# Kernel tuning notes

Hardware: AMD Instinct MI355X
Metric: run time of the kernel (lower is better)

The kernel has to match this reference:

```python
import jax, jax.numpy as jnp
import numpy as np

N = 131072  # time steps
D = 4       # SDE state dimension


def setup_inputs() -> dict:
    key = jax.random.key(0)
    k = jax.random.split(key, 6)
    F = 0.1 * jax.random.normal(k[0], (D, D), jnp.float32)  # only shape/dtype used by filter
    H = jnp.zeros((1, D), jnp.float32).at[0, 0].set(1.0)    # observe first state component
    P_inf = jnp.eye(D, dtype=jnp.float32)
    # stable per-step transitions: spectral radius ~0.9
    A_seq = 0.9 * jnp.eye(D, dtype=jnp.float32)[None] + 0.02 * jax.random.normal(k[1], (N, D, D), jnp.float32)
    # PSD process noise per step
    S = 0.05 * jax.random.normal(k[2], (N, D, D), jnp.float32)
    Q_seq = jnp.einsum('nij,nkj->nik', S, S) + 1e-3 * jnp.eye(D, dtype=jnp.float32)[None]
    residual = jax.random.normal(k[3], (N,), jnp.float32)   # y - mean_fn(times)
    mask = jnp.ones((N,), jnp.float32)                      # all steps observed
    R_seq = 0.1 + 0.05 * jax.random.uniform(k[4], (N,), jnp.float32)  # noise_var + floor
    return dict(F=F, H=H, P_inf=P_inf, A_seq=A_seq, Q_seq=Q_seq,
                residual=residual, mask=mask, R_seq=R_seq)


def _kalman_filter(F, H, P_inf, A_seq, Q_seq, residual, mask, R_seq):
    d = F.shape[0]
    eye = jnp.eye(d, dtype=F.dtype)
    h = H[0]  # (d,)
    log_2pi = jnp.log(2.0 * jnp.pi).astype(F.dtype)

    def step(carry, inputs):
        m, P = carry
        A, Q, r_n, mask_n, R_n = inputs
        m_pred = A @ m
        P_pred = A @ P @ A.T + Q
        P_pred = 0.5 * (P_pred + P_pred.T)
        Ph = P_pred @ h                 # (d,)
        S = h @ Ph + R_n                # innovation variance
        innov = r_n - h @ m_pred
        is_obs = mask_n == 1
        S_safe = jnp.where(is_obs, S, 1.0)
        K = jnp.where(is_obs, Ph / S_safe, jnp.zeros_like(Ph))
        m_new = m_pred + K * innov
        I_KH = eye - K[:, None] * h[None, :]
        P_new = I_KH @ P_pred @ I_KH.T + R_n * (K[:, None] * K[None, :])
        P_new = 0.5 * (P_new + P_new.T)
        ll = jnp.where(is_obs, -0.5 * (log_2pi + jnp.log(S_safe) + innov * innov / S_safe), 0.0)
        return (m_new, P_new), (m_pred, P_pred, m_new, P_new, ll)

    m0 = jnp.zeros(d, dtype=F.dtype)
    _, (m_pred_seq, P_pred_seq, m_filt_seq, P_filt_seq, ll_seq) = jax.lax.scan(
        step, (m0, P_inf), (A_seq, Q_seq, residual, mask, R_seq))
    return m_pred_seq, P_pred_seq, m_filt_seq, P_filt_seq, jnp.sum(ll_seq)


def _rts_smoother(m_pred_seq, P_pred_seq, m_filt_seq, P_filt_seq, A_seq):
    def step(carry, inputs):
        m_ns, P_ns = carry
        m_f, P_f, m_pn, P_pn, A_n = inputs
        J = jnp.linalg.solve(P_pn.T, A_n @ P_f.T).T
        m_s = m_f + J @ (m_ns - m_pn)
        P_s = P_f + J @ (P_ns - P_pn) @ J.T
        P_s = 0.5 * (P_s + P_s.T)
        return (m_s, P_s), (m_s, P_s)

    m_T = m_filt_seq[-1]
    P_T = P_filt_seq[-1]
    inputs = (m_filt_seq[:-1], P_filt_seq[:-1], m_pred_seq[1:], P_pred_seq[1:], A_seq[1:])
    _, (m_s, P_s) = jax.lax.scan(step, (m_T, P_T), inputs, reverse=True)
    return (jnp.concatenate([m_s, m_T[None]], axis=0),
            jnp.concatenate([P_s, P_T[None]], axis=0))


def reference(F, H, P_inf, A_seq, Q_seq, residual, mask, R_seq):
    m_pred, P_pred, m_filt, P_filt, log_marginal = _kalman_filter(
        F, H, P_inf, A_seq, Q_seq, residual, mask, R_seq)
    m_smooth, P_smooth = _rts_smoother(m_pred, P_pred, m_filt, P_filt, A_seq)
    h = H[0]
    means = m_smooth @ h                                   # (N,) observation-space means
    vars_ = jnp.einsum('i,nij,j->n', h, P_smooth, h)       # (N,) marginal variances
    return means, vars_, log_marginal
```

## Files before the change

### kernel.cpp

```cpp
#include <hip/hip_runtime.h>
#include <math.h>

#define NN 131072
#define WUP 32
#define TPB 320
#define NOUT 256
#define NBLK (NN / NOUT)
#define WIN 321
#define NREC 288
#define LOG2PI 1.8378770664093453f

typedef __attribute__((ext_vector_type(2))) float f2;

__device__ double g_llb[NBLK];

__device__ __forceinline__ f2 bc(float s) {
  f2 r = {s, s};
  return r;
}
#define PF(a, b, c) __builtin_elementwise_fma((a), (b), (c))

__device__ __forceinline__ void ldpk_flat(const float4* s, int stride, int w, f2* M) {
#pragma unroll
  for (int c = 0; c < 4; ++c) {
    float4 v = s[c * stride + w];
    M[2 * c] = f2{v.x, v.y};
    M[2 * c + 1] = f2{v.z, v.w};
  }
}

__device__ __forceinline__ void sym_rows(const float4 t0, const float4 t1, const float2 t2,
                                         f2* M) {
  M[0] = f2{t0.x, t0.y};
  M[1] = f2{t0.z, t0.w};
  M[2] = f2{t0.y, t1.x};
  M[3] = f2{t1.y, t1.z};
  M[4] = f2{t0.z, t1.y};
  M[5] = f2{t1.w, t2.x};
  M[6] = f2{t0.w, t1.z};
  M[7] = f2{t2.x, t2.y};
}

__device__ __forceinline__ void kf_step_pk(const f2* __restrict__ AT, const f2* __restrict__ Q,
                                           float r, float mk, float R, f2* __restrict__ m,
                                           f2* __restrict__ P, float& Ss, float& innov,
                                           bool& obs) {
  float m0 = m[0][0], m1 = m[0][1], m2_ = m[1][0], m3 = m[1][1];
  f2 mp[2];
#pragma unroll
  for (int p = 0; p < 2; ++p) {
    f2 acc = AT[p] * bc(m0);
    acc = PF(bc(m1), AT[2 + p], acc);
    acc = PF(bc(m2_), AT[4 + p], acc);
    acc = PF(bc(m3), AT[6 + p], acc);
    mp[p] = acc;
  }

  f2 T[8];
#pragma unroll
  for (int i = 0; i < 4; ++i) {
    float a0 = AT[0 + (i >> 1)][i & 1];
    float a1 = AT[2 + (i >> 1)][i & 1];
    float a2 = AT[4 + (i >> 1)][i & 1];
    float a3 = AT[6 + (i >> 1)][i & 1];
#pragma unroll
    for (int p = 0; p < 2; ++p) {
      f2 acc = P[p] * bc(a0);
      acc = PF(bc(a1), P[2 + p], acc);
      acc = PF(bc(a2), P[4 + p], acc);
      acc = PF(bc(a3), P[6 + p], acc);
      T[2 * i + p] = acc;
    }
  }

  f2 Pp[8];
#pragma unroll
  for (int i = 0; i < 4; ++i) {
    float t0 = T[2 * i][0], t1 = T[2 * i][1], t2 = T[2 * i + 1][0], t3 = T[2 * i + 1][1];
#pragma unroll
    for (int p = 0; p < 2; ++p) {
      f2 acc = PF(bc(t0), AT[p], Q[2 * i + p]);
      acc = PF(bc(t1), AT[2 + p], acc);
      acc = PF(bc(t2), AT[4 + p], acc);
      acc = PF(bc(t3), AT[6 + p], acc);
      Pp[2 * i + p] = acc;
    }
  }

  float S = Pp[0][0] + R;
  innov = r - mp[0][0];
  obs = (mk == 1.0f);
  Ss = obs ? S : 1.0f;
  float kf = obs ? __builtin_amdgcn_rcpf(S) : 0.0f;
  f2 K[2] = {Pp[0] * bc(kf), Pp[1] * bc(kf)};
#pragma unroll
  for (int p = 0; p < 2; ++p) m[p] = PF(K[p], bc(innov), mp[p]);

#pragma unroll
  for (int i = 0; i < 4; ++i) {
    float Ki = K[i >> 1][i & 1];
#pragma unroll
    for (int p = 0; p < 2; ++p) P[2 * i + p] = PF(bc(-Ki), Pp[p], Pp[2 * i + p]);
  }
}

__device__ __forceinline__ void chol_solve_pk(const f2* __restrict__ S, const f2* __restrict__ T,
                                              f2* __restrict__ X) {
  float s00 = S[0][0];
  float s10 = S[2][0], s11 = S[2][1];
  float s20 = S[4][0], s21 = S[4][1], s22 = S[5][0];
  float s30 = S[6][0], s31 = S[6][1], s32 = S[7][0], s33 = S[7][1];
  float i00 = __builtin_amdgcn_rsqf(s00);
  float l10 = s10 * i00, l20 = s20 * i00, l30 = s30 * i00;
  float i11 = __builtin_amdgcn_rsqf(s11 - l10 * l10);
  float l21 = (s21 - l20 * l10) * i11;
  float l31 = (s31 - l30 * l10) * i11;
  float i22 = __builtin_amdgcn_rsqf(s22 - l20 * l20 - l21 * l21);
  float l32 = (s32 - l30 * l20 - l31 * l21) * i22;
  float i33 = __builtin_amdgcn_rsqf(s33 - l30 * l30 - l31 * l31 - l32 * l32);
#pragma unroll
  for (int c = 0; c < 4; ++c) {
    float t0 = T[0 + (c >> 1)][c & 1];
    float t1 = T[2 + (c >> 1)][c & 1];
    float t2 = T[4 + (c >> 1)][c & 1];
    float t3 = T[6 + (c >> 1)][c & 1];
    float y0 = t0 * i00;
    float y1 = (t1 - l10 * y0) * i11;
    float y2 = (t2 - l20 * y0 - l21 * y1) * i22;
    float y3 = (t3 - l30 * y0 - l31 * y1 - l32 * y2) * i33;
    float x3 = y3 * i33;
    float x2 = (y2 - l32 * x3) * i22;
    float x1 = (y1 - l21 * x2 - l31 * x3) * i11;
    float x0 = (y0 - l10 * x1 - l20 * x2 - l30 * x3) * i00;
    X[0 + (c >> 1)][c & 1] = x0;
    X[2 + (c >> 1)][c & 1] = x1;
    X[4 + (c >> 1)][c & 1] = x2;
    X[6 + (c >> 1)][c & 1] = x3;
  }
}

__device__ __forceinline__ void make_record_reg(const f2* __restrict__ m,
                                                const f2* __restrict__ P,
                                                const f2* __restrict__ AT,
                                                const f2* __restrict__ Q, f2* __restrict__ X,
                                                f2* __restrict__ W, f2* __restrict__ u) {
  float m0 = m[0][0], m1 = m[0][1], m2_ = m[1][0], m3 = m[1][1];
  f2 pm[2];
#pragma unroll
  for (int p = 0; p < 2; ++p) {
    f2 acc = AT[p] * bc(m0);
    acc = PF(bc(m1), AT[2 + p], acc);
    acc = PF(bc(m2_), AT[4 + p], acc);
    acc = PF(bc(m3), AT[6 + p], acc);
    pm[p] = acc;
  }

  f2 T[8];
#pragma unroll
  for (int i = 0; i < 4; ++i) {
    float a0 = AT[0 + (i >> 1)][i & 1];
    float a1 = AT[2 + (i >> 1)][i & 1];
    float a2 = AT[4 + (i >> 1)][i & 1];
    float a3 = AT[6 + (i >> 1)][i & 1];
#pragma unroll
    for (int p = 0; p < 2; ++p) {
      f2 acc = P[p] * bc(a0);
      acc = PF(bc(a1), P[2 + p], acc);
      acc = PF(bc(a2), P[4 + p], acc);
      acc = PF(bc(a3), P[6 + p], acc);
      T[2 * i + p] = acc;
    }
  }

  f2 Ppn[8];
#pragma unroll
  for (int i = 0; i < 4; ++i) {
    float t0 = T[2 * i][0], t1 = T[2 * i][1], t2 = T[2 * i + 1][0], t3 = T[2 * i + 1][1];
#pragma unroll
    for (int p = 0; p < 2; ++p) {
      f2 acc = PF(bc(t0), AT[p], Q[2 * i + p]);
      acc = PF(bc(t1), AT[2 + p], acc);
      acc = PF(bc(t2), AT[4 + p], acc);
      acc = PF(bc(t3), AT[6 + p], acc);
      Ppn[2 * i + p] = acc;
    }
  }

  chol_solve_pk(Ppn, T, X);

  float p0 = pm[0][0], p1 = pm[0][1], p2 = pm[1][0], p3 = pm[1][1];
#pragma unroll
  for (int p = 0; p < 2; ++p) {
    f2 acc = X[p] * bc(p0);
    acc = PF(bc(p1), X[2 + p], acc);
    acc = PF(bc(p2), X[4 + p], acc);
    acc = PF(bc(p3), X[6 + p], acc);
    u[p] = m[p] - acc;
  }

  f2 Jp[8];
#pragma unroll
  for (int i = 0; i < 4; ++i) {
    float x0 = X[0 + (i >> 1)][i & 1];
    float x1 = X[2 + (i >> 1)][i & 1];
    float x2 = X[4 + (i >> 1)][i & 1];
    float x3 = X[6 + (i >> 1)][i & 1];
#pragma unroll
    for (int p = 0; p < 2; ++p) {
      f2 acc = Ppn[p] * bc(x0);
      acc = PF(bc(x1), Ppn[2 + p], acc);
      acc = PF(bc(x2), Ppn[4 + p], acc);
      acc = PF(bc(x3), Ppn[6 + p], acc);
      Jp[2 * i + p] = acc;
    }
  }
#pragma unroll
  for (int i = 0; i < 4; ++i) {
    float j0 = Jp[2 * i][0], j1 = Jp[2 * i][1], j2 = Jp[2 * i + 1][0], j3 = Jp[2 * i + 1][1];
#pragma unroll
    for (int p = 0; p < 2; ++p) {
      f2 acc = X[p] * bc(j0);
      acc = PF(bc(j1), X[2 + p], acc);
      acc = PF(bc(j2), X[4 + p], acc);
      acc = PF(bc(j3), X[6 + p], acc);
      W[2 * i + p] = P[2 * i + p] - acc;
    }
  }
}

__global__ __launch_bounds__(TPB, 1) void fused_kernel(const float* __restrict__ P_inf,
                                                       const float* __restrict__ A_seq,
                                                       const float* __restrict__ Q_seq,
                                                       const float* __restrict__ residual,
                                                       const float* __restrict__ mask,
                                                       const float* __restrict__ R_seq,
                                                       float* __restrict__ out) {
  __shared__ __align__(16) char smem[55040];
  __shared__ double sh[TPB];

  float4* sAT = (float4*)smem;
  float4* sQ0 = (float4*)(smem + 20544);
  float4* sQ1 = (float4*)(smem + 25680);
  float2* sQ2 = (float2*)(smem + 30816);
  float4* sRM = (float4*)(smem + 33384);
  float4* rJ = (float4*)smem;
  float4* rW0 = (float4*)(smem + 18432);
  float4* rW1 = (float4*)(smem + 23040);
  float2* rW2 = (float2*)(smem + 27648);
  float4* ru = (float4*)(smem + 29952);
  float4* fm = (float4*)(smem + 34560);
  float4* fP = (float4*)(smem + 38656);

  const int B = blockIdx.x * NOUT;
  const int t = threadIdx.x;
  const int base = B - WUP;

  const float4* Af4 = (const float4*)A_seq;
  const float4* Qf4 = (const float4*)Q_seq;
  for (int f = t; f < WIN * 4; f += TPB) {
    int w = f >> 2, c = f & 3;
    int k = base + w;
    k = k < 0 ? 0 : (k > NN - 1 ? NN - 1 : k);
    float4 rowA = Af4[(size_t)k * 4 + c];
    ((float*)&sAT[0 * WIN + w])[c] = rowA.x;
    ((float*)&sAT[1 * WIN + w])[c] = rowA.y;
    ((float*)&sAT[2 * WIN + w])[c] = rowA.z;
    ((float*)&sAT[3 * WIN + w])[c] = rowA.w;
    float4 rowQ = Qf4[(size_t)k * 4 + c];
    if (c == 0) {
      sQ0[w] = rowQ;
    } else if (c == 1) {
      sQ1[w].x = rowQ.y;
      sQ1[w].y = rowQ.z;
      sQ1[w].z = rowQ.w;
    } else if (c == 2) {
      sQ1[w].w = rowQ.z;
      sQ2[w].x = rowQ.w;
    } else {
      sQ2[w].y = rowQ.w;
    }
  }
  for (int w = t; w < WIN; w += TPB) {
    int k = base + w;
    k = k < 0 ? 0 : (k > NN - 1 ? NN - 1 : k);
    sRM[w] = make_float4(residual[k], R_seq[k], mask[k], 0.f);
  }
  __syncthreads();

  f2 m[2], P[8], X[8], W[8], u[2];
  float Ss = 1.f, innov = 0.f;
  bool obs = false;
  if (t < NREC) {
    int kown = B + t;
    if (kown > NN - 1) kown = NN - 1;
    int s0 = kown - WUP;
    if (s0 < 0) s0 = 0;

    m[0] = f2{0.f, 0.f};
    m[1] = f2{0.f, 0.f};
#pragma unroll
    for (int i = 0; i < 4; ++i) {
      P[2 * i] = f2{P_inf[i * 4 + 0], P_inf[i * 4 + 1]};
      P[2 * i + 1] = f2{P_inf[i * 4 + 2], P_inf[i * 4 + 3]};
    }

#pragma unroll 2
    for (int k = s0; k <= kown; ++k) {
      int w = k - base;
      f2 AT[8], Q[8];
      ldpk_flat(sAT, WIN, w, AT);
      sym_rows(sQ0[w], sQ1[w], sQ2[w], Q);
      float4 rm = sRM[w];
      kf_step_pk(AT, Q, rm.x, rm.z, rm.y, m, P, Ss, innov, obs);
    }

    int kn = kown + 1;
    if (kn > NN - 1) kn = NN - 1;
    int w = kn - base;
    f2 AT[8], Q[8];
    ldpk_flat(sAT, WIN, w, AT);
    sym_rows(sQ0[w], sQ1[w], sQ2[w], Q);
    make_record_reg(m, P, AT, Q, X, W, u);
  }

  sh[t] = (t < NOUT && obs) ? (double)(-0.5f * (LOG2PI + logf(Ss) + innov * innov / Ss)) : 0.0;
  __syncthreads();

  if (t < NREC) {
#pragma unroll
    for (int i = 0; i < 4; ++i)
      rJ[i * NREC + t] = make_float4(X[0 + (i >> 1)][i & 1], X[2 + (i >> 1)][i & 1],
                                     X[4 + (i >> 1)][i & 1], X[6 + (i >> 1)][i & 1]);
    rW0[t] = make_float4(W[0][0], W[0][1], W[1][0], W[1][1]);
    rW1[t] = make_float4(W[2][1], W[3][0], W[3][1], W[5][0]);
    rW2[t] = make_float2(W[5][1], W[7][1]);
    ru[t] = make_float4(u[0][0], u[0][1], u[1][0], u[1][1]);
    if (t >= WUP) {
      int j = t - WUP;
      fm[j] = make_float4(m[0][0], m[0][1], m[1][0], m[1][1]);
#pragma unroll
      for (int c = 0; c < 4; ++c)
        fP[c * NOUT + j] = make_float4(P[2 * c][0], P[2 * c][1], P[2 * c + 1][0], P[2 * c + 1][1]);
    }
  }

#pragma unroll
  for (int w = 128; w > 0; w >>= 1) {
    if (t < w) sh[t] += sh[t + w];
    __syncthreads();
  }
  if (t == 0) g_llb[blockIdx.x] = sh[0];

  if (t < NOUT) {
    const int n = B + t;
    int e = n + WUP;
    if (e > NN - 1) e = NN - 1;

    f2 r01 = f2{1.f, 0.f}, r23 = f2{0.f, 0.f};
    float alpha = 0.f, omega = 0.f;
#pragma unroll 2
    for (int k = n; k < e; ++k) {
      int w = k - B;
      float4 j0 = rJ[0 * NREC + w], j1 = rJ[1 * NREC + w];
      float4 j2 = rJ[2 * NREC + w], j3 = rJ[3 * NREC + w];
      f2 Wm[8];
      sym_rows(rW0[w], rW1[w], rW2[w], Wm);
      float4 uv = ru[w];
      float r0 = r01[0], r1 = r01[1], r2 = r23[0], r3 = r23[1];
      alpha += r0 * uv.x + r1 * uv.y + r2 * uv.z + r3 * uv.w;
      f2 s01 = Wm[0] * bc(r0);
      s01 = PF(bc(r1), Wm[2], s01);
      s01 = PF(bc(r2), Wm[4], s01);
      s01 = PF(bc(r3), Wm[6], s01);
      f2 s23 = Wm[1] * bc(r0);
      s23 = PF(bc(r1), Wm[3], s23);
      s23 = PF(bc(r2), Wm[5], s23);
      s23 = PF(bc(r3), Wm[7], s23);
      f2 os = r01 * s01;
      os = PF(r23, s23, os);
      omega += os[0] + os[1];
      f2 ja = f2{j0.x, j0.y}, jb = f2{j1.x, j1.y}, jc = f2{j2.x, j2.y}, jd = f2{j3.x, j3.y};
      f2 je = f2{j0.z, j0.w}, jf = f2{j1.z, j1.w}, jg = f2{j2.z, j2.w}, jh = f2{j3.z, j3.w};
      f2 n01 = ja * bc(r0);
      n01 = PF(bc(r1), jb, n01);
      n01 = PF(bc(r2), jc, n01);
      n01 = PF(bc(r3), jd, n01);
      f2 n23 = je * bc(r0);
      n23 = PF(bc(r1), jf, n23);
      n23 = PF(bc(r2), jg, n23);
      n23 = PF(bc(r3), jh, n23);
      r01 = n01;
      r23 = n23;
    }

    int j = e - B - WUP;
    float4 vm = fm[j];
    float r0 = r01[0], r1 = r01[1], r2 = r23[0], r3 = r23[1];
    float mean = alpha + r0 * vm.x + r1 * vm.y + r2 * vm.z + r3 * vm.w;
    float4 p0 = fP[0 * NOUT + j], p1 = fP[1 * NOUT + j];
    float4 p2 = fP[2 * NOUT + j], p3 = fP[3 * NOUT + j];
    float s0 = p0.x * r0 + p0.y * r1 + p0.z * r2 + p0.w * r3;
    float s1 = p1.x * r0 + p1.y * r1 + p1.z * r2 + p1.w * r3;
    float s2 = p2.x * r0 + p2.y * r1 + p2.z * r2 + p2.w * r3;
    float s3 = p3.x * r0 + p3.y * r1 + p3.z * r2 + p3.w * r3;
    float var = omega + r0 * s0 + r1 * s1 + r2 * s2 + r3 * s3;
    out[n] = mean;
    out[NN + n] = var;
  }
}

__global__ __launch_bounds__(256, 1) void llred_kernel(float* __restrict__ out) {
  __shared__ double sh[256];
  const int t = threadIdx.x;
  double acc = 0.0;
  for (int i = t; i < NBLK; i += 256) acc += g_llb[i];
  sh[t] = acc;
  __syncthreads();
#pragma unroll
  for (int w = 128; w > 0; w >>= 1) {
    if (t < w) sh[t] += sh[t + w];
    __syncthreads();
  }
  if (t == 0) out[2 * NN] = (float)sh[0];
}

extern "C" void kernel_launch(void* const* d_in, const int* in_sizes, int n_in, void* d_out,
                              int out_size, void* d_ws, size_t ws_size, hipStream_t stream) {
  const float* P_inf = (const float*)d_in[2];
  const float* A_seq = (const float*)d_in[3];
  const float* Q_seq = (const float*)d_in[4];
  const float* residual = (const float*)d_in[5];
  const float* mask = (const float*)d_in[6];
  const float* R_seq = (const float*)d_in[7];
  float* out = (float*)d_out;

  fused_kernel<<<NBLK, TPB, 0, stream>>>(P_inf, A_seq, Q_seq, residual, mask, R_seq, out);
  llred_kernel<<<1, 256, 0, stream>>>(out);
}
```

Before: 130.7 us.

## Stream smoother records through global memory and defer log-likelihood reduction

Per-step smoother records (gain J, covariance correction W, mean offset u) are now written straight to global arrays indexed by time step as soon as they are computed. The backward pass then reads them from global memory instead of from aliased shared memory. This frees the registers that held X, W and u across the barrier and removes the shared-memory aliasing. The block log-likelihood tree reduction moves after the smoother so it no longer delays it. In exchange, the backward loop pays global/L2 latency instead of LDS latency, and neighbouring blocks write overlapping record slots with identical values.

```diff
diff --git a/kernel.cpp b/kernel.cpp
--- a/kernel.cpp
+++ b/kernel.cpp
@@ -12,6 +12,11 @@
 
 typedef __attribute__((ext_vector_type(2))) float f2;
 
+__device__ float4 g_J[4][NN];
+__device__ float4 g_W0[NN];
+__device__ float4 g_W1[NN];
+__device__ float2 g_W2[NN];
+__device__ float4 g_u[NN];
 __device__ double g_llb[NBLK];
 
 __device__ __forceinline__ f2 bc(float s) {
@@ -19,15 +24,6 @@
   return r;
 }
 #define PF(a, b, c) __builtin_elementwise_fma((a), (b), (c))
-
-__device__ __forceinline__ void ldpk_flat(const float4* s, int stride, int w, f2* M) {
-#pragma unroll
-  for (int c = 0; c < 4; ++c) {
-    float4 v = s[c * stride + w];
-    M[2 * c] = f2{v.x, v.y};
-    M[2 * c + 1] = f2{v.z, v.w};
-  }
-}
 
 __device__ __forceinline__ void sym_rows(const float4 t0, const float4 t1, const float2 t2,
                                          f2* M) {
@@ -139,11 +135,10 @@
   }
 }
 
-__device__ __forceinline__ void make_record_reg(const f2* __restrict__ m,
-                                                const f2* __restrict__ P,
-                                                const f2* __restrict__ AT,
-                                                const f2* __restrict__ Q, f2* __restrict__ X,
-                                                f2* __restrict__ W, f2* __restrict__ u) {
+__device__ __forceinline__ void make_record_store(int n, const f2* __restrict__ m,
+                                                  const f2* __restrict__ P,
+                                                  const f2* __restrict__ AT,
+                                                  const f2* __restrict__ Q) {
   float m0 = m[0][0], m1 = m[0][1], m2_ = m[1][0], m3 = m[1][1];
   f2 pm[2];
 #pragma unroll
@@ -186,17 +181,31 @@
     }
   }
 
+  f2 X[8];
   chol_solve_pk(Ppn, T, X);
 
   float p0 = pm[0][0], p1 = pm[0][1], p2 = pm[1][0], p3 = pm[1][1];
-#pragma unroll
-  for (int p = 0; p < 2; ++p) {
-    f2 acc = X[p] * bc(p0);
-    acc = PF(bc(p1), X[2 + p], acc);
-    acc = PF(bc(p2), X[4 + p], acc);
-    acc = PF(bc(p3), X[6 + p], acc);
-    u[p] = m[p] - acc;
-  }
+  f2 u0, u1;
+  {
+    f2 acc = X[0] * bc(p0);
+    acc = PF(bc(p1), X[2], acc);
+    acc = PF(bc(p2), X[4], acc);
+    acc = PF(bc(p3), X[6], acc);
+    u0 = m[0] - acc;
+  }
+  {
+    f2 acc = X[1] * bc(p0);
+    acc = PF(bc(p1), X[3], acc);
+    acc = PF(bc(p2), X[5], acc);
+    acc = PF(bc(p3), X[7], acc);
+    u1 = m[1] - acc;
+  }
+  g_u[n] = make_float4(u0[0], u0[1], u1[0], u1[1]);
+
+#pragma unroll
+  for (int i = 0; i < 4; ++i)
+    g_J[i][n] = make_float4(X[0 + (i >> 1)][i & 1], X[2 + (i >> 1)][i & 1],
+                            X[4 + (i >> 1)][i & 1], X[6 + (i >> 1)][i & 1]);
 
   f2 Jp[8];
 #pragma unroll
@@ -214,6 +223,7 @@
       Jp[2 * i + p] = acc;
     }
   }
+  f2 W[8];
 #pragma unroll
   for (int i = 0; i < 4; ++i) {
     float j0 = Jp[2 * i][0], j1 = Jp[2 * i][1], j2 = Jp[2 * i + 1][0], j3 = Jp[2 * i + 1][1];
@@ -226,6 +236,9 @@
       W[2 * i + p] = P[2 * i + p] - acc;
     }
   }
+  g_W0[n] = make_float4(W[0][0], W[0][1], W[1][0], W[1][1]);
+  g_W1[n] = make_float4(W[2][1], W[3][0], W[3][1], W[5][0]);
+  g_W2[n] = make_float2(W[5][1], W[7][1]);
 }
 
 __global__ __launch_bounds__(TPB, 1) void fused_kernel(const float* __restrict__ P_inf,
@@ -235,21 +248,14 @@
                                                        const float* __restrict__ mask,
                                                        const float* __restrict__ R_seq,
                                                        float* __restrict__ out) {
-  __shared__ __align__(16) char smem[55040];
+  __shared__ float4 sAT[4][WIN];
+  __shared__ float4 sQ0[WIN];
+  __shared__ float4 sQ1[WIN];
+  __shared__ float2 sQ2[WIN];
+  __shared__ float4 sRM[WIN];
+  __shared__ float4 fm[NOUT];
+  __shared__ float4 fP[4][NOUT];
   __shared__ double sh[TPB];
-
-  float4* sAT = (float4*)smem;
-  float4* sQ0 = (float4*)(smem + 20544);
-  float4* sQ1 = (float4*)(smem + 25680);
-  float2* sQ2 = (float2*)(smem + 30816);
-  float4* sRM = (float4*)(smem + 33384);
-  float4* rJ = (float4*)smem;
-  float4* rW0 = (float4*)(smem + 18432);
-  float4* rW1 = (float4*)(smem + 23040);
-  float2* rW2 = (float2*)(smem + 27648);
-  float4* ru = (float4*)(smem + 29952);
-  float4* fm = (float4*)(smem + 34560);
-  float4* fP = (float4*)(smem + 38656);
 
   const int B = blockIdx.x * NOUT;
   const int t = threadIdx.x;
@@ -262,10 +268,10 @@
     int k = base + w;
     k = k < 0 ? 0 : (k > NN - 1 ? NN - 1 : k);
     float4 rowA = Af4[(size_t)k * 4 + c];
-    ((float*)&sAT[0 * WIN + w])[c] = rowA.x;
-    ((float*)&sAT[1 * WIN + w])[c] = rowA.y;
-    ((float*)&sAT[2 * WIN + w])[c] = rowA.z;
-    ((float*)&sAT[3 * WIN + w])[c] = rowA.w;
+    ((float*)&sAT[0][w])[c] = rowA.x;
+    ((float*)&sAT[1][w])[c] = rowA.y;
+    ((float*)&sAT[2][w])[c] = rowA.z;
+    ((float*)&sAT[3][w])[c] = rowA.w;
     float4 rowQ = Qf4[(size_t)k * 4 + c];
     if (c == 0) {
       sQ0[w] = rowQ;
@@ -287,7 +293,6 @@
   }
   __syncthreads();
 
-  f2 m[2], P[8], X[8], W[8], u[2];
   float Ss = 1.f, innov = 0.f;
   bool obs = false;
   if (t < NREC) {
@@ -296,8 +301,8 @@
     int s0 = kown - WUP;
     if (s0 < 0) s0 = 0;
 
-    m[0] = f2{0.f, 0.f};
-    m[1] = f2{0.f, 0.f};
+    f2 m[2] = {f2{0.f, 0.f}, f2{0.f, 0.f}};
+    f2 P[8];
 #pragma unroll
     for (int i = 0; i < 4; ++i) {
       P[2 * i] = f2{P_inf[i * 4 + 0], P_inf[i * 4 + 1]};
@@ -308,48 +313,41 @@
     for (int k = s0; k <= kown; ++k) {
       int w = k - base;
       f2 AT[8], Q[8];
-      ldpk_flat(sAT, WIN, w, AT);
+#pragma unroll
+      for (int c = 0; c < 4; ++c) {
+        float4 v = sAT[c][w];
+        AT[2 * c] = f2{v.x, v.y};
+        AT[2 * c + 1] = f2{v.z, v.w};
+      }
       sym_rows(sQ0[w], sQ1[w], sQ2[w], Q);
       float4 rm = sRM[w];
       kf_step_pk(AT, Q, rm.x, rm.z, rm.y, m, P, Ss, innov, obs);
+    }
+
+    if (t >= WUP) {
+      int j = t - WUP;
+      fm[j] = make_float4(m[0][0], m[0][1], m[1][0], m[1][1]);
+#pragma unroll
+      for (int c = 0; c < 4; ++c)
+        fP[c][j] = make_float4(P[2 * c][0], P[2 * c][1], P[2 * c + 1][0], P[2 * c + 1][1]);
     }
 
     int kn = kown + 1;
     if (kn > NN - 1) kn = NN - 1;
     int w = kn - base;
     f2 AT[8], Q[8];
-    ldpk_flat(sAT, WIN, w, AT);
+#pragma unroll
+    for (int c = 0; c < 4; ++c) {
+      float4 v = sAT[c][w];
+      AT[2 * c] = f2{v.x, v.y};
+      AT[2 * c + 1] = f2{v.z, v.w};
+    }
     sym_rows(sQ0[w], sQ1[w], sQ2[w], Q);
-    make_record_reg(m, P, AT, Q, X, W, u);
+    make_record_store(kown, m, P, AT, Q);
   }
 
   sh[t] = (t < NOUT && obs) ? (double)(-0.5f * (LOG2PI + logf(Ss) + innov * innov / Ss)) : 0.0;
   __syncthreads();
-
-  if (t < NREC) {
-#pragma unroll
-    for (int i = 0; i < 4; ++i)
-      rJ[i * NREC + t] = make_float4(X[0 + (i >> 1)][i & 1], X[2 + (i >> 1)][i & 1],
-                                     X[4 + (i >> 1)][i & 1], X[6 + (i >> 1)][i & 1]);
-    rW0[t] = make_float4(W[0][0], W[0][1], W[1][0], W[1][1]);
-    rW1[t] = make_float4(W[2][1], W[3][0], W[3][1], W[5][0]);
-    rW2[t] = make_float2(W[5][1], W[7][1]);
-    ru[t] = make_float4(u[0][0], u[0][1], u[1][0], u[1][1]);
-    if (t >= WUP) {
-      int j = t - WUP;
-      fm[j] = make_float4(m[0][0], m[0][1], m[1][0], m[1][1]);
-#pragma unroll
-      for (int c = 0; c < 4; ++c)
-        fP[c * NOUT + j] = make_float4(P[2 * c][0], P[2 * c][1], P[2 * c + 1][0], P[2 * c + 1][1]);
-    }
-  }
-
-#pragma unroll
-  for (int w = 128; w > 0; w >>= 1) {
-    if (t < w) sh[t] += sh[t + w];
-    __syncthreads();
-  }
-  if (t == 0) g_llb[blockIdx.x] = sh[0];
 
   if (t < NOUT) {
     const int n = B + t;
@@ -360,12 +358,10 @@
     float alpha = 0.f, omega = 0.f;
 #pragma unroll 2
     for (int k = n; k < e; ++k) {
-      int w = k - B;
-      float4 j0 = rJ[0 * NREC + w], j1 = rJ[1 * NREC + w];
-      float4 j2 = rJ[2 * NREC + w], j3 = rJ[3 * NREC + w];
+      float4 j0 = g_J[0][k], j1 = g_J[1][k], j2 = g_J[2][k], j3 = g_J[3][k];
       f2 Wm[8];
-      sym_rows(rW0[w], rW1[w], rW2[w], Wm);
-      float4 uv = ru[w];
+      sym_rows(g_W0[k], g_W1[k], g_W2[k], Wm);
+      float4 uv = g_u[k];
       float r0 = r01[0], r1 = r01[1], r2 = r23[0], r3 = r23[1];
       alpha += r0 * uv.x + r1 * uv.y + r2 * uv.z + r3 * uv.w;
       f2 s01 = Wm[0] * bc(r0);
@@ -397,8 +393,7 @@
     float4 vm = fm[j];
     float r0 = r01[0], r1 = r01[1], r2 = r23[0], r3 = r23[1];
     float mean = alpha + r0 * vm.x + r1 * vm.y + r2 * vm.z + r3 * vm.w;
-    float4 p0 = fP[0 * NOUT + j], p1 = fP[1 * NOUT + j];
-    float4 p2 = fP[2 * NOUT + j], p3 = fP[3 * NOUT + j];
+    float4 p0 = fP[0][j], p1 = fP[1][j], p2 = fP[2][j], p3 = fP[3][j];
     float s0 = p0.x * r0 + p0.y * r1 + p0.z * r2 + p0.w * r3;
     float s1 = p1.x * r0 + p1.y * r1 + p1.z * r2 + p1.w * r3;
     float s2 = p2.x * r0 + p2.y * r1 + p2.z * r2 + p2.w * r3;
@@ -407,6 +402,14 @@
     out[n] = mean;
     out[NN + n] = var;
   }
+
+#pragma unroll
+  for (int w = 128; w > 0; w >>= 1) {
+    __syncthreads();
+    if (t < w) sh[t] += sh[t + w];
+  }
+  __syncthreads();
+  if (t == 0) g_llb[blockIdx.x] = sh[0];
 }
 
 __global__ __launch_bounds__(256, 1) void llred_kernel(float* __restrict__ out) {
```

After: 142.3 us. 8.9% more time.
